# Kernel tuning notes

Hardware: AMD Instinct MI355X
Metric: run time of the kernel (lower is better)

Reference implementation:

```python
import jax, jax.numpy as jnp
import numpy as np

N, E, IN, HID, H, L, G = 20000, 320000, 128, 64, 4, 3, 128

def setup_inputs() -> dict:
    key = jax.random.key(0)
    ks = jax.random.split(key, 14)
    x = jax.random.normal(ks[0], (N, IN), dtype=jnp.float32)
    edge_index = jax.random.randint(ks[1], (2, E), 0, N, dtype=jnp.int64)
    batch = jnp.sort(jax.random.randint(ks[2], (N,), 0, G, dtype=jnp.int64))
    s_in = 1.0 / np.sqrt(IN)
    s_h = 1.0 / np.sqrt(HID)
    lin_W = jax.random.normal(ks[3], (IN, HID), jnp.float32) * s_in
    lin_b = jax.random.normal(ks[4], (HID,), jnp.float32) * 0.02
    Wq = jax.random.normal(ks[5], (L, HID, H * HID), jnp.float32) * s_h
    bq = jax.random.normal(ks[6], (L, H * HID), jnp.float32) * 0.02
    Wk = jax.random.normal(ks[7], (L, HID, H * HID), jnp.float32) * s_h
    bk = jax.random.normal(ks[8], (L, H * HID), jnp.float32) * 0.02
    Wv = jax.random.normal(ks[9], (L, HID, H * HID), jnp.float32) * s_h
    bv = jax.random.normal(ks[10], (L, H * HID), jnp.float32) * 0.02
    Ws = jax.random.normal(ks[11], (L, HID, HID), jnp.float32) * s_h
    bs = jax.random.normal(ks[12], (L, HID), jnp.float32) * 0.02
    return {"x": x, "edge_index": edge_index, "batch": batch,
            "lin_W": lin_W, "lin_b": lin_b, "Wq": Wq, "bq": bq,
            "Wk": Wk, "bk": bk, "Wv": Wv, "bv": bv, "Ws": Ws, "bs": bs}

def _transformer_conv(h, src, dst, Wq, bq, Wk, bk, Wv, bv, Ws, bs):
    # PyG TransformerConv(hid, hid, heads=H, concat=False), beta=False, root_weight=True
    n = h.shape[0]
    C = HID  # per-head dim
    q = (h @ Wq + bq).reshape(n, H, C)
    k = (h @ Wk + bk).reshape(n, H, C)
    v = (h @ Wv + bv).reshape(n, H, C)
    # per-edge attention logits: q_i . k_j / sqrt(C), i=dst (target), j=src
    alpha = jnp.einsum('ehc,ehc->eh', q[dst], k[src]) * (1.0 / np.sqrt(C))  # [E,H]
    # segment softmax over edges grouped by target node
    amax = jax.ops.segment_max(alpha, dst, num_segments=n)  # [N,H]
    amax = jnp.where(jnp.isfinite(amax), amax, 0.0)
    ex = jnp.exp(alpha - amax[dst])
    denom = jax.ops.segment_sum(ex, dst, num_segments=n)
    a = ex / jnp.maximum(denom[dst], 1e-16)  # [E,H]
    msg = a[:, :, None] * v[src]  # [E,H,C]
    agg = jax.ops.segment_sum(msg.reshape(-1, H * C), dst, num_segments=n)
    out = agg.reshape(n, H, C).mean(axis=1)  # concat=False -> head mean
    return out + h @ Ws + bs  # root/skip connection

def reference(x, edge_index, batch, lin_W, lin_b, Wq, bq, Wk, bk, Wv, bv, Ws, bs):
    src, dst = edge_index[0], edge_index[1]
    h = x @ lin_W + lin_b  # [N, HID]; dropout inactive in eval
    for l in range(L):
        h = jax.nn.relu(_transformer_conv(h, src, dst, Wq[l], bq[l], Wk[l], bk[l],
                                          Wv[l], bv[l], Ws[l], bs[l]))
    # global_add_pool: sum node features per graph
    return jax.ops.segment_sum(h, batch, num_segments=G)  # [G, HID]
```

## Files before the change

### kernel.cpp

```cpp
#include <hip/hip_runtime.h>
#include <math.h>

#define N_NODES 20000
#define N_EDGES 320000
#define DIM_IN 128
#define HID 64
#define HEADS 4
#define LAYERS 3
#define GRAPHS 128
#define HOP 68

typedef unsigned short ushort;
typedef ushort ushort8 __attribute__((ext_vector_type(8)));
typedef ushort ushort4v __attribute__((ext_vector_type(4)));
typedef short short8 __attribute__((ext_vector_type(8)));
typedef float f32x4 __attribute__((ext_vector_type(4)));

__device__ __forceinline__ float bf2f(ushort u) {
    return __uint_as_float(((unsigned int)u) << 16);
}
__device__ __forceinline__ ushort f2bf(float f) {
    unsigned int b = __float_as_uint(f);
    return (ushort)((b + 0x7FFFu + ((b >> 16) & 1u)) >> 16);
}


__global__ void hist_kernel(const int* __restrict__ dst, int* __restrict__ counts, int n) {
    int e = blockIdx.x * 256 + threadIdx.x;
    if (e < n) atomicAdd(&counts[dst[e]], 1);
}

__global__ __launch_bounds__(256) void blocksum_kernel(const int* __restrict__ counts,
                                                       int* __restrict__ bsum, int n) {
    int i = blockIdx.x * 256 + threadIdx.x;
    int v = (i < n) ? counts[i] : 0;
    int lane = threadIdx.x & 63, wave = threadIdx.x >> 6;
#pragma unroll
    for (int off = 32; off >= 1; off >>= 1) v += __shfl_xor(v, off);
    __shared__ int ws[4];
    if (lane == 0) ws[wave] = v;
    __syncthreads();
    if (threadIdx.x == 0) bsum[blockIdx.x] = ws[0] + ws[1] + ws[2] + ws[3];
}

__global__ __launch_bounds__(128) void scanb_kernel(const int* __restrict__ bsum,
                                                    int* __restrict__ bexcl, int nb) {
    int tid = threadIdx.x;
    int v = (tid < nb) ? bsum[tid] : 0;
    int lane = tid & 63, wave = tid >> 6;
    int s = v;
#pragma unroll
    for (int off = 1; off < 64; off <<= 1) {
        int t = __shfl_up(s, off);
        if (lane >= off) s += t;
    }
    __shared__ int w0sum;
    if (tid == 63) w0sum = s;
    __syncthreads();
    int excl = s - v + (wave ? w0sum : 0);
    if (tid < nb) bexcl[tid] = excl;
}

__global__ __launch_bounds__(256) void expand_kernel(const int* __restrict__ counts,
                                                     const int* __restrict__ bexcl,
                                                     int* __restrict__ offs,
                                                     int* __restrict__ cursor, int n) {
    int i = blockIdx.x * 256 + threadIdx.x;
    int v = (i < n) ? counts[i] : 0;
    int lane = threadIdx.x & 63, wave = threadIdx.x >> 6;
    int s = v;
#pragma unroll
    for (int off = 1; off < 64; off <<= 1) {
        int t = __shfl_up(s, off);
        if (lane >= off) s += t;
    }
    __shared__ int wsum[4];
    if (lane == 63) wsum[wave] = s;
    __syncthreads();
    int add = bexcl[blockIdx.x];
    for (int w = 0; w < wave; ++w) add += wsum[w];
    int excl = add + s - v;
    if (i < n) { offs[i] = excl; cursor[i] = excl; }
    if (i == 0) offs[n] = N_EDGES;
}

__global__ void scatter_kernel(const int* __restrict__ src, const int* __restrict__ dst,
                               int* __restrict__ cursor, int* __restrict__ csr, int n) {
    int e = blockIdx.x * 256 + threadIdx.x;
    if (e < n) {
        int d = dst[e];
        int pos = atomicAdd(&cursor[d], 1);
        csr[pos] = src[e];
    }
}


__global__ __launch_bounds__(256) void sortcnt_kernel(const int* __restrict__ offs,
                                                      int* __restrict__ degcnt,
                                                      int* __restrict__ rankbuf) {
    int i = blockIdx.x * 256 + threadIdx.x;
    if (i < N_NODES) {
        int deg = offs[i + 1] - offs[i];
        int key = 1023 - (deg < 1023 ? deg : 1023);
        rankbuf[i] = atomicAdd(&degcnt[key], 1);
    }
}

__global__ __launch_bounds__(1024) void scan1024_kernel(const int* __restrict__ degcnt,
                                                        int* __restrict__ degoff) {
    int tid = threadIdx.x;
    int v = degcnt[tid];
    int lane = tid & 63, wv = tid >> 6;
    int s = v;
#pragma unroll
    for (int off = 1; off < 64; off <<= 1) {
        int t = __shfl_up(s, off);
        if (lane >= off) s += t;
    }
    __shared__ int wsum[16];
    if (lane == 63) wsum[wv] = s;
    __syncthreads();
    int add = 0;
    for (int q = 0; q < wv; ++q) add += wsum[q];
    degoff[tid] = add + s - v;
}

__global__ __launch_bounds__(256) void sortscat_kernel(const int* __restrict__ offs,
                                                       const int* __restrict__ degoff,
                                                       const int* __restrict__ rankbuf,
                                                       int* __restrict__ perm) {
    int i = blockIdx.x * 256 + threadIdx.x;
    if (i < N_NODES) {
        int deg = offs[i + 1] - offs[i];
        int key = 1023 - (deg < 1023 ? deg : 1023);
        perm[degoff[key] + rankbuf[i]] = i;
    }
}


__global__ __launch_bounds__(256) void wcvt_all_kernel(
        const float* __restrict__ Wq, const float* __restrict__ bq,
        const float* __restrict__ Wk, const float* __restrict__ bk,
        const float* __restrict__ Wv, const float* __restrict__ bv,
        const float* __restrict__ Ws, const float* __restrict__ bs,
        const float* __restrict__ linW,
        ushort* __restrict__ Wt3, float* __restrict__ bias3,
        ushort* __restrict__ Wlt) {
    const int PER = 832 * 64;
    int idx = blockIdx.x * 256 + threadIdx.x;
    if (idx < 3 * PER) {
        int l = idx / PER;
        int r = idx - l * PER;
        int j = r >> 6, k = r & 63;
        const float* Wq_l = Wq + (size_t)l * HID * 256;
        const float* Wk_l = Wk + (size_t)l * HID * 256;
        const float* Wv_l = Wv + (size_t)l * HID * 256;
        const float* Ws_l = Ws + (size_t)l * HID * 64;
        float w;
        if (j < 256) {
            w = Wq_l[(size_t)k * 256 + j];
        } else if (j < 768) {
            int pout = j - 256;
            int isv = (pout >> 2) & 1;
            int low2 = pout & 3;
            int g = pout >> 3;
            int srccol = (g >> 4) * 64 + (g & 15) * 4 + low2;
            w = isv ? Wv_l[(size_t)k * 256 + srccol] : Wk_l[(size_t)k * 256 + srccol];
        } else {
            w = Ws_l[(size_t)k * 64 + (j - 768)];
        }
        Wt3[idx] = f2bf(w);
    } else {
        int idx2 = idx - 3 * PER;
        if (idx2 < 64 * DIM_IN) {
            int col = idx2 >> 7, k = idx2 & 127;
            Wlt[idx2] = f2bf(linW[(size_t)k * HID + col]);
        }
    }
    if (idx < 3 * 832) {
        int l = idx / 832, j = idx - l * 832;
        float b;
        if (j < 256) {
            b = bq[l * 256 + j];
        } else if (j < 768) {
            int pout = j - 256;
            int isv = (pout >> 2) & 1;
            int low2 = pout & 3;
            int g = pout >> 3;
            int srccol = (g >> 4) * 64 + (g & 15) * 4 + low2;
            b = isv ? bv[l * 256 + srccol] : bk[l * 256 + srccol];
        } else {
            b = bs[l * 64 + (j - 768)];
        }
        bias3[idx] = b;
    }
}


__device__ __forceinline__ void proj_rows(const float* __restrict__ ho,
        const ushort* __restrict__ Wt, const float* __restrict__ bias_cat,
        ushort* __restrict__ qsb, ushort* __restrict__ kvp,
        int grow, bool ok, int lane, int t0, int tstep) {
    int lr = lane & 15;
    int koff = (lane >> 4) * 8;
    short8 bh[2];
#pragma unroll
    for (int mm = 0; mm < 2; ++mm) {
        const float* hp = ho + lr * HOP + mm * 32 + koff;
        float4 f0 = *(const float4*)hp;
        float4 f1 = *(const float4*)(hp + 4);
        ushort8 u;
        u[0] = f2bf(f0.x); u[1] = f2bf(f0.y); u[2] = f2bf(f0.z); u[3] = f2bf(f0.w);
        u[4] = f2bf(f1.x); u[5] = f2bf(f1.y); u[6] = f2bf(f1.z); u[7] = f2bf(f1.w);
        bh[mm] = __builtin_bit_cast(short8, u);
    }
    for (int t = t0; t < 52; t += tstep) {
        const ushort* wb = Wt + (size_t)(t * 16 + lr) * HID + koff;
        short8 w0 = *(const short8*)wb;
        short8 w1 = *(const short8*)(wb + 32);
        f32x4 a_ = (f32x4){0.f, 0.f, 0.f, 0.f};
        a_ = __builtin_amdgcn_mfma_f32_16x16x32_bf16(w0, bh[0], a_, 0, 0, 0);
        a_ = __builtin_amdgcn_mfma_f32_16x16x32_bf16(w1, bh[1], a_, 0, 0, 0);
        int j = t * 16 + ((lane >> 4) << 2);
        float4 bs4 = *(const float4*)(bias_cat + j);
        ushort4v u4;
        u4[0] = f2bf(a_[0] + bs4.x);
        u4[1] = f2bf(a_[1] + bs4.y);
        u4[2] = f2bf(a_[2] + bs4.z);
        u4[3] = f2bf(a_[3] + bs4.w);
        if (ok) {
            ushort* dst;
            if (j < 256)      dst = qsb + (size_t)grow * 320 + j;
            else if (j < 768) dst = kvp + (size_t)grow * 512 + (j - 256);
            else              dst = qsb + (size_t)grow * 320 + 256 + (j - 768);
            *(ushort4v*)dst = u4;
        }
    }
}


__global__ __launch_bounds__(256) void linproj_kernel(const float* __restrict__ x,
        const ushort* __restrict__ Wlt, const float* __restrict__ lb,
        const ushort* __restrict__ Wt0, const float* __restrict__ bias0,
        ushort* __restrict__ qsb, ushort* __restrict__ kvp) {
    __shared__ float ho[64 * HOP];
    int tid = threadIdx.x;
    int w = tid >> 6, l = tid & 63;
    int r0 = blockIdx.x * 64 + w * 16;
    int row = r0 + (l & 15);
    int rowc = (row < N_NODES) ? row : (N_NODES - 1);

    short8 a[4];
#pragma unroll
    for (int kc = 0; kc < 4; ++kc) {
        const float* xp = x + (size_t)rowc * DIM_IN + kc * 32 + (l >> 4) * 8;
        float4 f0 = *(const float4*)xp;
        float4 f1 = *(const float4*)(xp + 4);
        ushort8 u;
        u[0] = f2bf(f0.x); u[1] = f2bf(f0.y); u[2] = f2bf(f0.z); u[3] = f2bf(f0.w);
        u[4] = f2bf(f1.x); u[5] = f2bf(f1.y); u[6] = f2bf(f1.z); u[7] = f2bf(f1.w);
        a[kc] = __builtin_bit_cast(short8, u);
    }

    f32x4 acc[4];
#pragma unroll
    for (int t = 0; t < 4; ++t) acc[t] = (f32x4){0.f, 0.f, 0.f, 0.f};

    const ushort* wb = Wlt + (size_t)(l & 15) * DIM_IN + (l >> 4) * 8;
#pragma unroll
    for (int t = 0; t < 4; ++t) {
#pragma unroll
        for (int kc = 0; kc < 4; ++kc) {
            short8 b = *(const short8*)(wb + (size_t)t * 16 * DIM_IN + kc * 32);
            acc[t] = __builtin_amdgcn_mfma_f32_16x16x32_bf16(b, a[kc], acc[t], 0, 0, 0);
        }
    }

    float* hrow = ho + (size_t)(w * 16 + (l & 15)) * HOP;
#pragma unroll
    for (int t = 0; t < 4; ++t) {
        int j = t * 16 + ((l >> 4) << 2);
        float4 bias = *(const float4*)(lb + j);
        float4 o;
        o.x = acc[t][0] + bias.x;
        o.y = acc[t][1] + bias.y;
        o.z = acc[t][2] + bias.z;
        o.w = acc[t][3] + bias.w;
        *(float4*)(hrow + j) = o;
    }
    proj_rows(ho + (size_t)w * 16 * HOP, Wt0, bias0, qsb, kvp,
              row, row < N_NODES, l, 0, 1);
}


__device__ __forceinline__ float4 attn_node(int node, int lane,
        const ushort* __restrict__ qsb, const ushort8* __restrict__ kvp,
        const int* __restrict__ offs, const int* __restrict__ csr) {
    int hh = lane >> 4;
    int cb = (lane & 15) * 4;
    const ushort* nb = qsb + (size_t)node * 320;
    ushort4v qu = *(const ushort4v*)(nb + hh * 64 + cb);
    float qx = bf2f(qu[0]), qy = bf2f(qu[1]), qz = bf2f(qu[2]), qw = bf2f(qu[3]);

    const float SCL = 0.125f * 1.44269504088896340736f;
    float m = -INFINITY, l = 0.f;
    float4 acc = make_float4(0.f, 0.f, 0.f, 0.f);

    int e0 = offs[node], e1 = offs[node + 1];
    int cnt = e1 - e0;

    ushort8 cur = (ushort8)(0);
    ushort8 nxt = (ushort8)(0);
    if (cnt > 0) cur = kvp[(size_t)csr[e0] * 64 + lane];
    if (cnt > 1) nxt = kvp[(size_t)csr[e0 + 1] * 64 + lane];

    for (int i = 0; i < cnt; ++i) {
        ushort8 u = cur;
        cur = nxt;
        if (i + 2 < cnt) nxt = kvp[(size_t)csr[e0 + i + 2] * 64 + lane];

        float p = qx * bf2f(u[0]) + qy * bf2f(u[1]) + qz * bf2f(u[2]) + qw * bf2f(u[3]);
        p += __shfl_xor(p, 1);
        p += __shfl_xor(p, 2);
        p += __shfl_xor(p, 4);
        p += __shfl_xor(p, 8);
        float alpha = p * SCL;
        if (__any(alpha > m)) {
            float nm = fmaxf(m, alpha);
            float sc = exp2f(m - nm);
            l *= sc; acc.x *= sc; acc.y *= sc; acc.z *= sc; acc.w *= sc;
            m = nm;
        }
        float pe = exp2f(alpha - m);
        l += pe;
        acc.x += pe * bf2f(u[4]);
        acc.y += pe * bf2f(u[5]);
        acc.z += pe * bf2f(u[6]);
        acc.w += pe * bf2f(u[7]);
    }

    float inv = (l > 0.f) ? (1.f / l) : 0.f;
    float4 r;
    r.x = acc.x * inv;
    r.y = acc.y * inv;
    r.z = acc.z * inv;
    r.w = acc.w * inv;
    r.x += __shfl_xor(r.x, 16); r.x += __shfl_xor(r.x, 32);
    r.y += __shfl_xor(r.y, 16); r.y += __shfl_xor(r.y, 32);
    r.z += __shfl_xor(r.z, 16); r.z += __shfl_xor(r.z, 32);
    r.w += __shfl_xor(r.w, 16); r.w += __shfl_xor(r.w, 32);

    ushort4v su = *(const ushort4v*)(nb + 256 + cb);
    float4 o;
    o.x = fmaxf(r.x * 0.25f + bf2f(su[0]), 0.f);
    o.y = fmaxf(r.y * 0.25f + bf2f(su[1]), 0.f);
    o.z = fmaxf(r.z * 0.25f + bf2f(su[2]), 0.f);
    o.w = fmaxf(r.w * 0.25f + bf2f(su[3]), 0.f);
    return o;
}


__global__ __launch_bounds__(1024) void edgeproj_kernel(const ushort* __restrict__ qsb_in,
        const ushort8* __restrict__ kvp_in,
        const int* __restrict__ offs, const int* __restrict__ csr,
        const int* __restrict__ perm,
        const ushort* __restrict__ Wt_next, const float* __restrict__ bias_next,
        ushort* __restrict__ qsb_out, ushort* __restrict__ kvp_out) {
    __shared__ float ho[16 * HOP];
    int tid = threadIdx.x;
    int w = tid >> 6, l = tid & 63;
    int node = perm[blockIdx.x * 16 + w];
    float4 o = attn_node(node, l, qsb_in, kvp_in, offs, csr);
    if ((l >> 4) == 0)
        *(float4*)(ho + (size_t)w * HOP + (l & 15) * 4) = o;
    __syncthreads();
    int grow = perm[blockIdx.x * 16 + (l & 15)];
    proj_rows(ho, Wt_next, bias_next, qsb_out, kvp_out, grow, true, l, w, 16);
}


__global__ __launch_bounds__(256) void edge_kernel(const ushort* __restrict__ qsb,
        const ushort8* __restrict__ kvp,
        const int* __restrict__ offs, const int* __restrict__ csr,
        float* __restrict__ hout) {
    int w = threadIdx.x >> 6, l = threadIdx.x & 63;
    int node = blockIdx.x * 4 + w;
    float4 o = attn_node(node, l, qsb, kvp, offs, csr);
    if ((l >> 4) == 0)
        *(float4*)(hout + (size_t)node * HID + (l & 15) * 4) = o;
}


__global__ __launch_bounds__(256) void pool_kernel(const float* __restrict__ h,
                                                   const int* __restrict__ batch,
                                                   float* __restrict__ out) {
    int g = blockIdx.x;
    int lo = 0, hi = N_NODES;
    while (lo < hi) { int mid = (lo + hi) >> 1; if (batch[mid] < g) lo = mid + 1; else hi = mid; }
    int start = lo;
    hi = N_NODES;
    while (lo < hi) { int mid = (lo + hi) >> 1; if (batch[mid] < g + 1) lo = mid + 1; else hi = mid; }
    int end = lo;
    int c = threadIdx.x & 63;
    int sub = threadIdx.x >> 6;
    float acc = 0.f;
    for (int i = start + sub; i < end; i += 4) acc += h[(size_t)i * HID + c];
    __shared__ float lds[4][64];
    lds[sub][c] = acc;
    __syncthreads();
    if (sub == 0) out[g * HID + c] = lds[0][c] + lds[1][c] + lds[2][c] + lds[3][c];
}


extern "C" void kernel_launch(void* const* d_in, const int* in_sizes, int n_in,
                              void* d_out, int out_size, void* d_ws, size_t ws_size,
                              hipStream_t stream) {
    const float* x    = (const float*)d_in[0];
    const int*   edge = (const int*)d_in[1];
    const int*   batch= (const int*)d_in[2];
    const float* linW = (const float*)d_in[3];
    const float* linb = (const float*)d_in[4];
    const float* Wq   = (const float*)d_in[5];
    const float* bq   = (const float*)d_in[6];
    const float* Wk   = (const float*)d_in[7];
    const float* bk   = (const float*)d_in[8];
    const float* Wv   = (const float*)d_in[9];
    const float* bv   = (const float*)d_in[10];
    const float* Ws   = (const float*)d_in[11];
    const float* bs   = (const float*)d_in[12];
    float* out = (float*)d_out;

    const int* src = edge;
    const int* dst = edge + N_EDGES;

    ushort* qsb0 = (ushort*)d_ws;
    ushort* qsb1 = qsb0 + (size_t)N_NODES * 320;
    ushort* kvp0 = qsb1 + (size_t)N_NODES * 320;
    ushort* kvp1 = kvp0 + (size_t)N_NODES * 512;
    float*  h3   = (float*)kvp1;
    int* counts = (int*)(kvp1 + (size_t)N_NODES * 512);
    int* degcnt = counts + N_NODES;
    int* offs   = degcnt + 1024;
    int* cursor = offs + N_NODES + 1;
    int* csr    = cursor + N_NODES;
    int* bsum   = csr + N_EDGES;
    int* bexcl  = bsum + 128;
    int* degoff = bexcl + 128;
    int* rankbuf= degoff + 1024;
    int* perm   = rankbuf + N_NODES;
    ushort* Wt3 = (ushort*)(perm + N_NODES);
    float* bias3 = (float*)(Wt3 + 3 * 832 * 64);
    ushort* Wlt = (ushort*)(bias3 + 3 * 832);

    const int NB = (N_NODES + 255) / 256;

    hipMemsetAsync(counts, 0, (N_NODES + 1024) * sizeof(int), stream);
    hist_kernel<<<(N_EDGES + 255) / 256, 256, 0, stream>>>(dst, counts, N_EDGES);
    blocksum_kernel<<<NB, 256, 0, stream>>>(counts, bsum, N_NODES);
    scanb_kernel<<<1, 128, 0, stream>>>(bsum, bexcl, NB);
    expand_kernel<<<NB, 256, 0, stream>>>(counts, bexcl, offs, cursor, N_NODES);
    scatter_kernel<<<(N_EDGES + 255) / 256, 256, 0, stream>>>(src, dst, cursor, csr, N_EDGES);

    sortcnt_kernel<<<NB, 256, 0, stream>>>(offs, degcnt, rankbuf);
    scan1024_kernel<<<1, 1024, 0, stream>>>(degcnt, degoff);
    sortscat_kernel<<<NB, 256, 0, stream>>>(offs, degoff, rankbuf, perm);

    wcvt_all_kernel<<<(3 * 832 * 64 + 64 * DIM_IN + 255) / 256, 256, 0, stream>>>(
        Wq, bq, Wk, bk, Wv, bv, Ws, bs, linW, Wt3, bias3, Wlt);

    linproj_kernel<<<(N_NODES + 63) / 64, 256, 0, stream>>>(
        x, Wlt, linb, Wt3, bias3, qsb0, kvp0);

    edgeproj_kernel<<<N_NODES / 16, 1024, 0, stream>>>(
        qsb0, (const ushort8*)kvp0, offs, csr, perm,
        Wt3 + (size_t)1 * 832 * 64, bias3 + 832, qsb1, kvp1);

    edgeproj_kernel<<<N_NODES / 16, 1024, 0, stream>>>(
        qsb1, (const ushort8*)kvp1, offs, csr, perm,
        Wt3 + (size_t)2 * 832 * 64, bias3 + 1664, qsb0, kvp0);

    edge_kernel<<<N_NODES / 4, 256, 0, stream>>>(
        qsb0, (const ushort8*)kvp0, offs, csr, h3);

    pool_kernel<<<GRAPHS, 256, 0, stream>>>(h3, batch, out);
}
```

Before: 430.5 us.

## Fuse CSR build, degree sort, weight conversion and pooling into fewer launches

Merges the edge histogram with the weight conversion, block sums with the degree-bucket count, the two scans into one kernel, and expand with the permutation scatter. Degrees are now read from counts instead of offs. The final attention kernel adds its outputs straight into the pooled result with atomics, which removes the h3 buffer and the separate pool kernel. This cuts about six launches and one intermediate pass, at the cost of atomic contention on the 128x64 output and a nondeterministic float summation order.

```diff
diff --git a/kernel.cpp b/kernel.cpp
--- a/kernel.cpp
+++ b/kernel.cpp
@@ -25,120 +25,8 @@
 }
 
 
-__global__ void hist_kernel(const int* __restrict__ dst, int* __restrict__ counts, int n) {
-    int e = blockIdx.x * 256 + threadIdx.x;
-    if (e < n) atomicAdd(&counts[dst[e]], 1);
-}
-
-__global__ __launch_bounds__(256) void blocksum_kernel(const int* __restrict__ counts,
-                                                       int* __restrict__ bsum, int n) {
-    int i = blockIdx.x * 256 + threadIdx.x;
-    int v = (i < n) ? counts[i] : 0;
-    int lane = threadIdx.x & 63, wave = threadIdx.x >> 6;
-#pragma unroll
-    for (int off = 32; off >= 1; off >>= 1) v += __shfl_xor(v, off);
-    __shared__ int ws[4];
-    if (lane == 0) ws[wave] = v;
-    __syncthreads();
-    if (threadIdx.x == 0) bsum[blockIdx.x] = ws[0] + ws[1] + ws[2] + ws[3];
-}
-
-__global__ __launch_bounds__(128) void scanb_kernel(const int* __restrict__ bsum,
-                                                    int* __restrict__ bexcl, int nb) {
-    int tid = threadIdx.x;
-    int v = (tid < nb) ? bsum[tid] : 0;
-    int lane = tid & 63, wave = tid >> 6;
-    int s = v;
-#pragma unroll
-    for (int off = 1; off < 64; off <<= 1) {
-        int t = __shfl_up(s, off);
-        if (lane >= off) s += t;
-    }
-    __shared__ int w0sum;
-    if (tid == 63) w0sum = s;
-    __syncthreads();
-    int excl = s - v + (wave ? w0sum : 0);
-    if (tid < nb) bexcl[tid] = excl;
-}
-
-__global__ __launch_bounds__(256) void expand_kernel(const int* __restrict__ counts,
-                                                     const int* __restrict__ bexcl,
-                                                     int* __restrict__ offs,
-                                                     int* __restrict__ cursor, int n) {
-    int i = blockIdx.x * 256 + threadIdx.x;
-    int v = (i < n) ? counts[i] : 0;
-    int lane = threadIdx.x & 63, wave = threadIdx.x >> 6;
-    int s = v;
-#pragma unroll
-    for (int off = 1; off < 64; off <<= 1) {
-        int t = __shfl_up(s, off);
-        if (lane >= off) s += t;
-    }
-    __shared__ int wsum[4];
-    if (lane == 63) wsum[wave] = s;
-    __syncthreads();
-    int add = bexcl[blockIdx.x];
-    for (int w = 0; w < wave; ++w) add += wsum[w];
-    int excl = add + s - v;
-    if (i < n) { offs[i] = excl; cursor[i] = excl; }
-    if (i == 0) offs[n] = N_EDGES;
-}
-
-__global__ void scatter_kernel(const int* __restrict__ src, const int* __restrict__ dst,
-                               int* __restrict__ cursor, int* __restrict__ csr, int n) {
-    int e = blockIdx.x * 256 + threadIdx.x;
-    if (e < n) {
-        int d = dst[e];
-        int pos = atomicAdd(&cursor[d], 1);
-        csr[pos] = src[e];
-    }
-}
-
-
-__global__ __launch_bounds__(256) void sortcnt_kernel(const int* __restrict__ offs,
-                                                      int* __restrict__ degcnt,
-                                                      int* __restrict__ rankbuf) {
-    int i = blockIdx.x * 256 + threadIdx.x;
-    if (i < N_NODES) {
-        int deg = offs[i + 1] - offs[i];
-        int key = 1023 - (deg < 1023 ? deg : 1023);
-        rankbuf[i] = atomicAdd(&degcnt[key], 1);
-    }
-}
-
-__global__ __launch_bounds__(1024) void scan1024_kernel(const int* __restrict__ degcnt,
-                                                        int* __restrict__ degoff) {
-    int tid = threadIdx.x;
-    int v = degcnt[tid];
-    int lane = tid & 63, wv = tid >> 6;
-    int s = v;
-#pragma unroll
-    for (int off = 1; off < 64; off <<= 1) {
-        int t = __shfl_up(s, off);
-        if (lane >= off) s += t;
-    }
-    __shared__ int wsum[16];
-    if (lane == 63) wsum[wv] = s;
-    __syncthreads();
-    int add = 0;
-    for (int q = 0; q < wv; ++q) add += wsum[q];
-    degoff[tid] = add + s - v;
-}
-
-__global__ __launch_bounds__(256) void sortscat_kernel(const int* __restrict__ offs,
-                                                       const int* __restrict__ degoff,
-                                                       const int* __restrict__ rankbuf,
-                                                       int* __restrict__ perm) {
-    int i = blockIdx.x * 256 + threadIdx.x;
-    if (i < N_NODES) {
-        int deg = offs[i + 1] - offs[i];
-        int key = 1023 - (deg < 1023 ? deg : 1023);
-        perm[degoff[key] + rankbuf[i]] = i;
-    }
-}
-
-
-__global__ __launch_bounds__(256) void wcvt_all_kernel(
+__global__ __launch_bounds__(256) void histwcvt_kernel(
+        const int* __restrict__ dst, int* __restrict__ counts,
         const float* __restrict__ Wq, const float* __restrict__ bq,
         const float* __restrict__ Wk, const float* __restrict__ bk,
         const float* __restrict__ Wv, const float* __restrict__ bv,
@@ -148,6 +36,7 @@
         ushort* __restrict__ Wlt) {
     const int PER = 832 * 64;
     int idx = blockIdx.x * 256 + threadIdx.x;
+    if (idx < N_EDGES) atomicAdd(&counts[dst[idx]], 1);
     if (idx < 3 * PER) {
         int l = idx / PER;
         int r = idx - l * PER;
@@ -170,12 +59,10 @@
             w = Ws_l[(size_t)k * 64 + (j - 768)];
         }
         Wt3[idx] = f2bf(w);
-    } else {
+    } else if (idx < 3 * PER + 64 * DIM_IN) {
         int idx2 = idx - 3 * PER;
-        if (idx2 < 64 * DIM_IN) {
-            int col = idx2 >> 7, k = idx2 & 127;
-            Wlt[idx2] = f2bf(linW[(size_t)k * HID + col]);
-        }
+        int col = idx2 >> 7, k = idx2 & 127;
+        Wlt[idx2] = f2bf(linW[(size_t)k * HID + col]);
     }
     if (idx < 3 * 832) {
         int l = idx / 832, j = idx - l * 832;
@@ -193,6 +80,104 @@
             b = bs[l * 64 + (j - 768)];
         }
         bias3[idx] = b;
+    }
+}
+
+
+__global__ __launch_bounds__(256) void blocksum_sortcnt_kernel(const int* __restrict__ counts,
+        int* __restrict__ bsum, int* __restrict__ degcnt, int* __restrict__ rankbuf) {
+    int i = blockIdx.x * 256 + threadIdx.x;
+    int v = (i < N_NODES) ? counts[i] : 0;
+    if (i < N_NODES) {
+        int key = 1023 - (v < 1023 ? v : 1023);
+        rankbuf[i] = atomicAdd(&degcnt[key], 1);
+    }
+    int lane = threadIdx.x & 63, wave = threadIdx.x >> 6;
+    int s = v;
+#pragma unroll
+    for (int off = 32; off >= 1; off >>= 1) s += __shfl_xor(s, off);
+    __shared__ int ws[4];
+    if (lane == 0) ws[wave] = s;
+    __syncthreads();
+    if (threadIdx.x == 0) bsum[blockIdx.x] = ws[0] + ws[1] + ws[2] + ws[3];
+}
+
+
+__global__ __launch_bounds__(1024) void scans_kernel(const int* __restrict__ degcnt,
+        int* __restrict__ degoff, const int* __restrict__ bsum, int* __restrict__ bexcl,
+        int nb) {
+    int tid = threadIdx.x;
+    int v = degcnt[tid];
+    int lane = tid & 63, wv = tid >> 6;
+    int s = v;
+#pragma unroll
+    for (int off = 1; off < 64; off <<= 1) {
+        int t = __shfl_up(s, off);
+        if (lane >= off) s += t;
+    }
+    __shared__ int wsum[16];
+    if (lane == 63) wsum[wv] = s;
+    __syncthreads();
+    int add = 0;
+    for (int q = 0; q < wv; ++q) add += wsum[q];
+    degoff[tid] = add + s - v;
+    if (tid < 64) {
+        int v0 = (tid < nb) ? bsum[tid] : 0;
+        int s0 = v0;
+#pragma unroll
+        for (int off = 1; off < 64; off <<= 1) {
+            int t = __shfl_up(s0, off);
+            if (lane >= off) s0 += t;
+        }
+        int carry = __shfl(s0, 63);
+        int v1 = (tid + 64 < nb) ? bsum[tid + 64] : 0;
+        int s1 = v1;
+#pragma unroll
+        for (int off = 1; off < 64; off <<= 1) {
+            int t = __shfl_up(s1, off);
+            if (lane >= off) s1 += t;
+        }
+        if (tid < nb) bexcl[tid] = s0 - v0;
+        if (tid + 64 < nb) bexcl[tid + 64] = carry + s1 - v1;
+    }
+}
+
+
+__global__ __launch_bounds__(256) void expand_sortscat_kernel(const int* __restrict__ counts,
+        const int* __restrict__ bexcl, int* __restrict__ offs, int* __restrict__ cursor,
+        const int* __restrict__ degoff, const int* __restrict__ rankbuf,
+        int* __restrict__ perm) {
+    int i = blockIdx.x * 256 + threadIdx.x;
+    int v = (i < N_NODES) ? counts[i] : 0;
+    int lane = threadIdx.x & 63, wave = threadIdx.x >> 6;
+    int s = v;
+#pragma unroll
+    for (int off = 1; off < 64; off <<= 1) {
+        int t = __shfl_up(s, off);
+        if (lane >= off) s += t;
+    }
+    __shared__ int wsum[4];
+    if (lane == 63) wsum[wave] = s;
+    __syncthreads();
+    int add = bexcl[blockIdx.x];
+    for (int w = 0; w < wave; ++w) add += wsum[w];
+    int excl = add + s - v;
+    if (i < N_NODES) {
+        offs[i] = excl;
+        cursor[i] = excl;
+        int key = 1023 - (v < 1023 ? v : 1023);
+        perm[degoff[key] + rankbuf[i]] = i;
+    }
+    if (i == 0) offs[N_NODES] = N_EDGES;
+}
+
+__global__ void scatter_kernel(const int* __restrict__ src, const int* __restrict__ dst,
+                               int* __restrict__ cursor, int* __restrict__ csr, int n) {
+    int e = blockIdx.x * 256 + threadIdx.x;
+    if (e < n) {
+        int d = dst[e];
+        int pos = atomicAdd(&cursor[d], 1);
+        csr[pos] = src[e];
     }
 }
 
@@ -379,36 +364,21 @@
 }
 
 
-__global__ __launch_bounds__(256) void edge_kernel(const ushort* __restrict__ qsb,
+__global__ __launch_bounds__(256) void edgepool_kernel(const ushort* __restrict__ qsb,
         const ushort8* __restrict__ kvp,
         const int* __restrict__ offs, const int* __restrict__ csr,
-        float* __restrict__ hout) {
+        const int* __restrict__ batch, float* __restrict__ out) {
     int w = threadIdx.x >> 6, l = threadIdx.x & 63;
     int node = blockIdx.x * 4 + w;
     float4 o = attn_node(node, l, qsb, kvp, offs, csr);
-    if ((l >> 4) == 0)
-        *(float4*)(hout + (size_t)node * HID + (l & 15) * 4) = o;
-}
-
-
-__global__ __launch_bounds__(256) void pool_kernel(const float* __restrict__ h,
-                                                   const int* __restrict__ batch,
-                                                   float* __restrict__ out) {
-    int g = blockIdx.x;
-    int lo = 0, hi = N_NODES;
-    while (lo < hi) { int mid = (lo + hi) >> 1; if (batch[mid] < g) lo = mid + 1; else hi = mid; }
-    int start = lo;
-    hi = N_NODES;
-    while (lo < hi) { int mid = (lo + hi) >> 1; if (batch[mid] < g + 1) lo = mid + 1; else hi = mid; }
-    int end = lo;
-    int c = threadIdx.x & 63;
-    int sub = threadIdx.x >> 6;
-    float acc = 0.f;
-    for (int i = start + sub; i < end; i += 4) acc += h[(size_t)i * HID + c];
-    __shared__ float lds[4][64];
-    lds[sub][c] = acc;
-    __syncthreads();
-    if (sub == 0) out[g * HID + c] = lds[0][c] + lds[1][c] + lds[2][c] + lds[3][c];
+    if ((l >> 4) == 0) {
+        int g = batch[node];
+        float* op = out + (size_t)g * HID + (l & 15) * 4;
+        atomicAdd(op + 0, o.x);
+        atomicAdd(op + 1, o.y);
+        atomicAdd(op + 2, o.z);
+        atomicAdd(op + 3, o.w);
+    }
 }
 
 
@@ -437,7 +407,6 @@
     ushort* qsb1 = qsb0 + (size_t)N_NODES * 320;
     ushort* kvp0 = qsb1 + (size_t)N_NODES * 320;
     ushort* kvp1 = kvp0 + (size_t)N_NODES * 512;
-    float*  h3   = (float*)kvp1;
     int* counts = (int*)(kvp1 + (size_t)N_NODES * 512);
     int* degcnt = counts + N_NODES;
     int* offs   = degcnt + 1024;
@@ -455,18 +424,19 @@
     const int NB = (N_NODES + 255) / 256;
 
     hipMemsetAsync(counts, 0, (N_NODES + 1024) * sizeof(int), stream);
-    hist_kernel<<<(N_EDGES + 255) / 256, 256, 0, stream>>>(dst, counts, N_EDGES);
-    blocksum_kernel<<<NB, 256, 0, stream>>>(counts, bsum, N_NODES);
-    scanb_kernel<<<1, 128, 0, stream>>>(bsum, bexcl, NB);
-    expand_kernel<<<NB, 256, 0, stream>>>(counts, bexcl, offs, cursor, N_NODES);
+    hipMemsetAsync(out, 0, (size_t)GRAPHS * HID * sizeof(float), stream);
+
+    histwcvt_kernel<<<(N_EDGES + 255) / 256, 256, 0, stream>>>(
+        dst, counts, Wq, bq, Wk, bk, Wv, bv, Ws, bs, linW, Wt3, bias3, Wlt);
+
+    blocksum_sortcnt_kernel<<<NB, 256, 0, stream>>>(counts, bsum, degcnt, rankbuf);
+
+    scans_kernel<<<1, 1024, 0, stream>>>(degcnt, degoff, bsum, bexcl, NB);
+
+    expand_sortscat_kernel<<<NB, 256, 0, stream>>>(counts, bexcl, offs, cursor,
+                                                   degoff, rankbuf, perm);
+
     scatter_kernel<<<(N_EDGES + 255) / 256, 256, 0, stream>>>(src, dst, cursor, csr, N_EDGES);
-
-    sortcnt_kernel<<<NB, 256, 0, stream>>>(offs, degcnt, rankbuf);
-    scan1024_kernel<<<1, 1024, 0, stream>>>(degcnt, degoff);
-    sortscat_kernel<<<NB, 256, 0, stream>>>(offs, degoff, rankbuf, perm);
-
-    wcvt_all_kernel<<<(3 * 832 * 64 + 64 * DIM_IN + 255) / 256, 256, 0, stream>>>(
-        Wq, bq, Wk, bk, Wv, bv, Ws, bs, linW, Wt3, bias3, Wlt);
 
     linproj_kernel<<<(N_NODES + 63) / 64, 256, 0, stream>>>(
         x, Wlt, linb, Wt3, bias3, qsb0, kvp0);
@@ -479,8 +449,6 @@
         qsb1, (const ushort8*)kvp1, offs, csr, perm,
         Wt3 + (size_t)2 * 832 * 64, bias3 + 1664, qsb0, kvp0);
 
-    edge_kernel<<<N_NODES / 4, 256, 0, stream>>>(
-        qsb0, (const ushort8*)kvp0, offs, csr, h3);
-
-    pool_kernel<<<GRAPHS, 256, 0, stream>>>(h3, batch, out);
-}
+    edgepool_kernel<<<N_NODES / 4, 256, 0, stream>>>(
+        qsb0, (const ushort8*)kvp0, offs, csr, batch, out);
+}
```

Result: slower. 443.5 us (+3.0%).
